# Performance work log

Measured on AMD Instinct MI355X. Metric: run time of the kernel, lower is better.

The kernel has to match this reference:

```python
import jax, jax.numpy as jnp
import numpy as np

N, D, H = 50000, 256, 8
HD = D // H
E = 800000
NEG_SLOPE = 0.2


def setup_inputs() -> dict:
    key = jax.random.key(0)
    ks = jax.random.split(key, 12)
    s = 1.0 / np.sqrt(D)
    return {
        "x": jax.random.normal(ks[0], (N, D), jnp.float32),
        "edge_index": jax.random.randint(ks[1], (2, E), 0, N, jnp.int64),
        "edge_attr": jax.random.normal(ks[2], (E, 16), jnp.float32),
        # GATConv params: lin weight (no bias), attention vectors, output bias
        "W": jax.random.normal(ks[3], (D, D), jnp.float32) * s,
        "att_src": jax.random.normal(ks[4], (H, HD), jnp.float32) * s,
        "att_dst": jax.random.normal(ks[5], (H, HD), jnp.float32) * s,
        "bias": jnp.zeros((D,), jnp.float32),
        # LayerNorm
        "ln_g": jnp.ones((D,), jnp.float32),
        "ln_b": jnp.zeros((D,), jnp.float32),
        # FFN
        "W1": jax.random.normal(ks[6], (D, D), jnp.float32) * s,
        "b1": jnp.zeros((D,), jnp.float32),
        "W2": jax.random.normal(ks[7], (D, D), jnp.float32) * s,
        "b2": jnp.zeros((D,), jnp.float32),
    }


def _gat_layer(x, edge_index, W, att_src, att_dst, bias, ln_g, ln_b, W1, b1, W2, b2):
    n = x.shape[0]
    # GATConv default add_self_loops=True
    sl = jnp.arange(n, dtype=edge_index.dtype)
    src = jnp.concatenate([edge_index[0], sl])  # [E+N]
    dst = jnp.concatenate([edge_index[1], sl])  # [E+N]

    xp = (x @ W).reshape(n, H, HD)                      # [N,H,hd]
    a_src = jnp.einsum("nhd,hd->nh", xp, att_src)        # [N,H]
    a_dst = jnp.einsum("nhd,hd->nh", xp, att_dst)        # [N,H]

    e = a_src[src] + a_dst[dst]                          # [E+N,H]
    e = jax.nn.leaky_relu(e, NEG_SLOPE)
    # segment softmax over destination nodes (every node has a self loop)
    m = jax.ops.segment_max(e, dst, num_segments=n)      # [N,H]
    ex = jnp.exp(e - m[dst])
    denom = jax.ops.segment_sum(ex, dst, num_segments=n) # [N,H]
    alpha = ex / (denom[dst] + 1e-16)                    # [E+N,H]

    msg = alpha[:, :, None] * xp[src]                    # [E+N,H,hd]
    out = jax.ops.segment_sum(msg, dst, num_segments=n)  # [N,H,hd]
    h = out.reshape(n, D) + bias

    # residual + LayerNorm
    r = h + x
    mu = jnp.mean(r, axis=-1, keepdims=True)
    var = jnp.mean(jnp.square(r - mu), axis=-1, keepdims=True)
    hn = (r - mu) / jnp.sqrt(var + 1e-5) * ln_g + ln_b

    # FFN
    return jax.nn.relu(hn @ W1 + b1) @ W2 + b2


def reference(x, edge_index, edge_attr, W, att_src, att_dst, bias, ln_g, ln_b, W1, b1, W2, b2):
    # edge_attr is accepted but unused (GATConv built without edge_dim)
    return _gat_layer(x, edge_index, W, att_src, att_dst, bias, ln_g, ln_b, W1, b1, W2, b2)
```

## Files before the change

kernel.cpp:

```cpp
#include <hip/hip_runtime.h>
#include <hip/hip_bf16.h>

#define H 8
#define HD 32
#define DD 256
#define NEG_SLOPE 0.2f
#define EPB 4096
#define NBMAX 256

typedef short bf16x8 __attribute__((ext_vector_type(8)));
typedef float f32x4 __attribute__((ext_vector_type(4)));

__device__ __forceinline__ unsigned short f2bf(float f) {
    unsigned int u = __float_as_uint(f);
    unsigned int r = (u + 0x7fffu + ((u >> 16) & 1u)) >> 16;
    return (unsigned short)r;
}
__device__ __forceinline__ float bf2f(unsigned short b) {
    return __uint_as_float(((unsigned int)b) << 16);
}

#define GLOAD_LDS16(g, s)                                                        \
    __builtin_amdgcn_global_load_lds((const __attribute__((address_space(1))) void*)(g), \
                                     (__attribute__((address_space(3))) void*)(s), 16, 0, 0)

__global__ __launch_bounds__(256) void zero_gc(int* __restrict__ gc) {
    gc[threadIdx.x] = 0;
}

__global__ __launch_bounds__(256) void prep(const float* __restrict__ x, unsigned short* __restrict__ xb,
                                            const float* __restrict__ W, unsigned short* __restrict__ Wt,
                                            const float* __restrict__ W1, unsigned short* __restrict__ W1t,
                                            const float* __restrict__ W2, unsigned short* __restrict__ W2t,
                                            const int* __restrict__ ei, int* __restrict__ gc,
                                            int* __restrict__ blockBase, int N, int n4, int E, int SB) {
    __shared__ int lhist[NBMAX];
    int b = blockIdx.x;
    int tid = threadIdx.x;
    if (b < SB) {
        lhist[tid] = 0;
        __syncthreads();
        int e0 = b * EPB;
#pragma unroll
        for (int i = 0; i < 16; i++) {
            int e = e0 + i * 256 + tid;
            if (e < E) atomicAdd(&lhist[((unsigned)ei[E + e]) >> 8], 1);
        }
        __syncthreads();
        int c = lhist[tid];
        blockBase[b * NBMAX + tid] = c ? atomicAdd(&gc[tid], c) : 0;
    } else if (b < SB + 768) {
        int wb = b - SB;
        const float* src = (wb < 256) ? W : (wb < 512) ? W1 : W2;
        unsigned short* dst = (wb < 256) ? Wt : (wb < 512) ? W1t : W2t;
        int i = (wb & 255) * 256 + tid;
        int n = i >> 8, k = i & 255;
        dst[i] = f2bf(src[k * 256 + n]);
    } else {
        int i = (b - SB - 768) * 256 + tid;
        if (i < n4) {
            float4 v = ((const float4*)x)[i];
            ushort4 o;
            o.x = f2bf(v.x); o.y = f2bf(v.y); o.z = f2bf(v.z); o.w = f2bf(v.w);
            ((ushort4*)xb)[i] = o;
        }
    }
}

__global__ __launch_bounds__(64) void scan_gc(const int* __restrict__ gc, int* __restrict__ bb) {
    int lane = threadIdx.x;
    int v[4], s = 0;
#pragma unroll
    for (int i = 0; i < 4; i++) { v[i] = gc[lane * 4 + i]; s += v[i]; }
    int sc = s;
#pragma unroll
    for (int off = 1; off < 64; off <<= 1) {
        int t = __shfl_up(sc, off, 64);
        if (lane >= off) sc += t;
    }
    int run = sc - s;
#pragma unroll
    for (int i = 0; i < 4; i++) { bb[lane * 4 + i] = run; run += v[i]; }
}

__global__ __launch_bounds__(256) void bucket_scatter(const int* __restrict__ ei,
                                                      const int* __restrict__ bb,
                                                      const int* __restrict__ blockBase,
                                                      unsigned int* __restrict__ tmp, int E) {
    __shared__ int lrank[NBMAX];
    int b = blockIdx.x;
    int tid = threadIdx.x;
    lrank[tid] = 0;
    __syncthreads();
    int e0 = b * EPB;
#pragma unroll
    for (int i = 0; i < 16; i++) {
        int e = e0 + i * 256 + tid;
        if (e < E) {
            int s = ei[e];
            unsigned d = (unsigned)ei[E + e];
            int k = d >> 8;
            int r = atomicAdd(&lrank[k], 1);
            tmp[bb[k] + blockBase[b * NBMAX + k] + r] = ((d & 255u) << 24) | (unsigned)s;
        }
    }
}

__global__ __launch_bounds__(256) void bucket_csr(const unsigned int* __restrict__ tmp,
                                                  const int* __restrict__ bb, const int* __restrict__ gc,
                                                  int* __restrict__ src_sorted, int* __restrict__ rowPtr,
                                                  int* __restrict__ cnt, int N) {
    __shared__ int dh[NBMAX];
    __shared__ int dbase[NBMAX];
    __shared__ int dr[NBMAX];
    int k = blockIdx.x;
    int tid = threadIdx.x;
    int base = bb[k];
    int M = gc[k];
    dh[tid] = 0;
    dr[tid] = 0;
    __syncthreads();
    for (int i = tid; i < M; i += 256) atomicAdd(&dh[tmp[base + i] >> 24], 1);
    __syncthreads();
    int c = dh[tid];
    dbase[tid] = c;
    __syncthreads();
    for (int off = 1; off < 256; off <<= 1) {
        int add = (tid >= off) ? dbase[tid - off] : 0;
        __syncthreads();
        dbase[tid] += add;
        __syncthreads();
    }
    int excl = dbase[tid] - c;
    int d = (k << 8) + tid;
    if (d < N) { cnt[d] = c; rowPtr[d] = base + excl; }
    __syncthreads();
    dbase[tid] = excl;
    __syncthreads();
    for (int i = tid; i < M; i += 256) {
        unsigned p = tmp[base + i];
        int dl = p >> 24;
        int r = atomicAdd(&dr[dl], 1);
        src_sorted[base + dbase[dl] + r] = (int)(p & 0xFFFFFFu);
    }
}

template <bool ATTN, bool PHASE2>
__global__ __launch_bounds__(256) void gemm_fused(
    const unsigned short* __restrict__ A,
    const unsigned short* __restrict__ B1t, const float* __restrict__ b1,
    const unsigned short* __restrict__ B2t, const float* __restrict__ b2,
    void* __restrict__ Cout, int M,
    const float* __restrict__ att_s, const float* __restrict__ att_d,
    float* __restrict__ a_srcO, float* __restrict__ a_dstO) {
    __shared__ __align__(16) unsigned short Als[16384];
    __shared__ __align__(16) unsigned short t1ls[PHASE2 ? 64 * 280 : 8];

    const int tid = threadIdx.x;
    const int l = tid & 63;
    const int w = tid >> 6;
    const int r16 = l & 15, q0 = l >> 4;
    const int row0 = blockIdx.x * 64;

#pragma unroll
    for (int k = 0; k < 8; k++) {
        int c = k * 256 + tid;
        const unsigned short* g = A + (size_t)min(row0 + (c & 63), M - 1) * DD + (c >> 6) * 8;
        GLOAD_LDS16(g, &Als[c * 8]);
    }
    __syncthreads();

    f32x4 zero = {0.f, 0.f, 0.f, 0.f};
    f32x4 acc[4][4];
#pragma unroll
    for (int i = 0; i < 4; i++)
#pragma unroll
        for (int j = 0; j < 4; j++) acc[i][j] = zero;

#pragma unroll
    for (int kk = 0; kk < 4; kk++) {
#pragma unroll
        for (int t = 0; t < 2; t++) {
            const int qq = kk * 8 + t * 4 + q0;
            bf16x8 af[4], bf[4];
#pragma unroll
            for (int j = 0; j < 4; j++)
                bf[j] = *(const bf16x8*)&B1t[(size_t)(w * 64 + j * 16 + r16) * DD + qq * 8];
#pragma unroll
            for (int i = 0; i < 4; i++)
                af[i] = *(const bf16x8*)&Als[(qq * 64 + i * 16 + r16) * 8];
#pragma unroll
            for (int i = 0; i < 4; i++)
#pragma unroll
                for (int j = 0; j < 4; j++)
                    acc[i][j] = __builtin_amdgcn_mfma_f32_16x16x32_bf16(af[i], bf[j], acc[i][j], 0, 0, 0);
        }
    }

    if (!PHASE2) {
        float aws0, aws1, aws2, aws3, awd0, awd1, awd2, awd3;
        int hA = 0, hB = 0;
        if (ATTN) {
            hA = w * 2; hB = hA + 1;
            aws0 = att_s[hA * HD + r16];
            aws1 = att_s[hA * HD + 16 + r16];
            aws2 = att_s[hB * HD + r16];
            aws3 = att_s[hB * HD + 16 + r16];
            awd0 = att_d[hA * HD + r16];
            awd1 = att_d[hA * HD + 16 + r16];
            awd2 = att_d[hB * HD + r16];
            awd3 = att_d[hB * HD + 16 + r16];
        }
#pragma unroll
        for (int i = 0; i < 4; i++) {
#pragma unroll
            for (int r = 0; r < 4; r++) {
                int row = row0 + i * 16 + q0 * 4 + r;
                if (row < M) {
#pragma unroll
                    for (int j = 0; j < 4; j++) {
                        int col = w * 64 + j * 16 + r16;
                        ((unsigned short*)Cout)[(size_t)row * DD + col] = f2bf(acc[i][j][r]);
                    }
                }
                if (ATTN) {
                    float v0 = acc[i][0][r], v1 = acc[i][1][r];
                    float v2 = acc[i][2][r], v3 = acc[i][3][r];
                    float ps0 = v0 * aws0 + v1 * aws1;
                    float ps1 = v2 * aws2 + v3 * aws3;
                    float pd0 = v0 * awd0 + v1 * awd1;
                    float pd1 = v2 * awd2 + v3 * awd3;
#pragma unroll
                    for (int m = 1; m < 16; m <<= 1) {
                        ps0 += __shfl_xor(ps0, m, 64);
                        ps1 += __shfl_xor(ps1, m, 64);
                        pd0 += __shfl_xor(pd0, m, 64);
                        pd1 += __shfl_xor(pd1, m, 64);
                    }
                    if (r16 == 0 && row < M) {
                        a_srcO[row * H + hA] = ps0;
                        a_srcO[row * H + hB] = ps1;
                        a_dstO[row * H + hA] = pd0;
                        a_dstO[row * H + hB] = pd1;
                    }
                }
            }
        }
    } else {
        float bb1[4];
#pragma unroll
        for (int j = 0; j < 4; j++) bb1[j] = b1[w * 64 + j * 16 + r16];
#pragma unroll
        for (int i = 0; i < 4; i++)
#pragma unroll
            for (int r = 0; r < 4; r++) {
                int rl = i * 16 + q0 * 4 + r;
#pragma unroll
                for (int j = 0; j < 4; j++) {
                    float v = fmaxf(acc[i][j][r] + bb1[j], 0.f);
                    t1ls[rl * 280 + w * 64 + j * 16 + r16] = f2bf(v);
                }
            }
        __syncthreads();

#pragma unroll
        for (int i = 0; i < 4; i++)
#pragma unroll
            for (int j = 0; j < 4; j++) acc[i][j] = zero;

#pragma unroll
        for (int kk = 0; kk < 4; kk++) {
#pragma unroll
            for (int t = 0; t < 2; t++) {
                const int qq = kk * 8 + t * 4 + q0;
                bf16x8 af[4], bf[4];
#pragma unroll
                for (int j = 0; j < 4; j++)
                    bf[j] = *(const bf16x8*)&B2t[(size_t)(w * 64 + j * 16 + r16) * DD + qq * 8];
#pragma unroll
                for (int i = 0; i < 4; i++)
                    af[i] = *(const bf16x8*)&t1ls[(i * 16 + r16) * 280 + qq * 8];
#pragma unroll
                for (int i = 0; i < 4; i++)
#pragma unroll
                    for (int j = 0; j < 4; j++)
                        acc[i][j] = __builtin_amdgcn_mfma_f32_16x16x32_bf16(af[i], bf[j], acc[i][j], 0, 0, 0);
            }
        }

        float bb2[4];
#pragma unroll
        for (int j = 0; j < 4; j++) bb2[j] = b2[w * 64 + j * 16 + r16];
#pragma unroll
        for (int i = 0; i < 4; i++)
#pragma unroll
            for (int r = 0; r < 4; r++) {
                int row = row0 + i * 16 + q0 * 4 + r;
                if (row < M) {
#pragma unroll
                    for (int j = 0; j < 4; j++) {
                        int col = w * 64 + j * 16 + r16;
                        ((float*)Cout)[(size_t)row * DD + col] = acc[i][j][r] + bb2[j];
                    }
                }
            }
    }
}

__global__ __launch_bounds__(256) void aggregate_ln(
    const unsigned short* __restrict__ xp, const unsigned short* __restrict__ x_bf,
    const float* __restrict__ a_src, const float* __restrict__ a_dst,
    const int* __restrict__ rowPtr, const int* __restrict__ cnt,
    const int* __restrict__ src_sorted,
    const float* __restrict__ bias, const float* __restrict__ ln_g,
    const float* __restrict__ ln_b, unsigned short* __restrict__ hn, int N) {
    int wave = threadIdx.x >> 6;
    int lane = threadIdx.x & 63;
    int n = blockIdx.x * 4 + wave;
    if (n >= N) return;
    int h = lane >> 3;

    float adst = a_dst[n * H + h];
    float e0 = a_src[n * H + h] + adst;
    e0 = (e0 > 0.f) ? e0 : NEG_SLOPE * e0;
    float ex = __expf(e0);
    ushort4 u = *(const ushort4*)(xp + (size_t)n * DD + lane * 4);
    float acc0 = ex * bf2f(u.x), acc1 = ex * bf2f(u.y);
    float acc2 = ex * bf2f(u.z), acc3 = ex * bf2f(u.w);
    float denom = ex;

    int beg = rowPtr[n];
    int end = beg + cnt[n];
    int i = beg;
    for (; i + 7 < end; i += 8) {
        int s[8];
        float es[8];
        ushort4 uu[8];
#pragma unroll
        for (int k = 0; k < 8; k++) s[k] = src_sorted[i + k];
#pragma unroll
        for (int k = 0; k < 8; k++) es[k] = a_src[s[k] * H + h];
#pragma unroll
        for (int k = 0; k < 8; k++) uu[k] = *(const ushort4*)(xp + (size_t)s[k] * DD + lane * 4);
#pragma unroll
        for (int k = 0; k < 8; k++) {
            float e = es[k] + adst;
            e = (e > 0.f) ? e : NEG_SLOPE * e;
            float wk = __expf(e);
            acc0 += wk * bf2f(uu[k].x);
            acc1 += wk * bf2f(uu[k].y);
            acc2 += wk * bf2f(uu[k].z);
            acc3 += wk * bf2f(uu[k].w);
            denom += wk;
        }
    }
    for (; i < end; i++) {
        int s0 = src_sorted[i];
        float es0 = a_src[s0 * H + h];
        ushort4 u0 = *(const ushort4*)(xp + (size_t)s0 * DD + lane * 4);
        float e0a = es0 + adst;
        e0a = (e0a > 0.f) ? e0a : NEG_SLOPE * e0a;
        float w0 = __expf(e0a);
        acc0 += w0 * bf2f(u0.x);
        acc1 += w0 * bf2f(u0.y);
        acc2 += w0 * bf2f(u0.z);
        acc3 += w0 * bf2f(u0.w);
        denom += w0;
    }
    float inv = 1.f / (denom + 1e-16f);
    float4 bb = *(const float4*)(bias + lane * 4);
    ushort4 xr = *(const ushort4*)(x_bf + (size_t)n * DD + lane * 4);
    float r0 = acc0 * inv + bb.x + bf2f(xr.x);
    float r1 = acc1 * inv + bb.y + bf2f(xr.y);
    float r2 = acc2 * inv + bb.z + bf2f(xr.z);
    float r3 = acc3 * inv + bb.w + bf2f(xr.w);

    float s = r0 + r1 + r2 + r3;
#pragma unroll
    for (int m = 1; m < 64; m <<= 1) s += __shfl_xor(s, m, 64);
    float mu = s * (1.f / 256.f);
    float d0 = r0 - mu, d1 = r1 - mu, d2 = r2 - mu, d3 = r3 - mu;
    float qv = d0 * d0 + d1 * d1 + d2 * d2 + d3 * d3;
#pragma unroll
    for (int m = 1; m < 64; m <<= 1) qv += __shfl_xor(qv, m, 64);
    float rstd = rsqrtf(qv * (1.f / 256.f) + 1e-5f);
    float4 g = *(const float4*)(ln_g + lane * 4);
    float4 b = *(const float4*)(ln_b + lane * 4);
    ushort4 o;
    o.x = f2bf(d0 * rstd * g.x + b.x);
    o.y = f2bf(d1 * rstd * g.y + b.y);
    o.z = f2bf(d2 * rstd * g.z + b.z);
    o.w = f2bf(d3 * rstd * g.w + b.w);
    *(ushort4*)(hn + (size_t)n * DD + lane * 4) = o;
}

extern "C" void kernel_launch(void* const* d_in, const int* in_sizes, int n_in,
                              void* d_out, int out_size, void* d_ws, size_t ws_size,
                              hipStream_t stream) {
    const float* x = (const float*)d_in[0];
    const int* edge_index = (const int*)d_in[1];
    const float* W = (const float*)d_in[3];
    const float* att_src = (const float*)d_in[4];
    const float* att_dst = (const float*)d_in[5];
    const float* bias = (const float*)d_in[6];
    const float* ln_g = (const float*)d_in[7];
    const float* ln_b = (const float*)d_in[8];
    const float* W1 = (const float*)d_in[9];
    const float* b1 = (const float*)d_in[10];
    const float* W2 = (const float*)d_in[11];
    const float* b2 = (const float*)d_in[12];

    const int N = in_sizes[0] / DD;
    const int E = in_sizes[1] / 2;

    char* p = (char*)d_ws;
    auto carve = [&](size_t bytes) {
        char* r = p;
        p += (bytes + 255) & ~(size_t)255;
        return r;
    };
    unsigned short* x_bf = (unsigned short*)carve((size_t)N * DD * 2);
    unsigned short* xp_bf = (unsigned short*)carve((size_t)N * DD * 2);
    unsigned short* hn_bf = (unsigned short*)carve((size_t)N * DD * 2);
    float* a_src = (float*)carve((size_t)N * H * 4);
    float* a_dst = (float*)carve((size_t)N * H * 4);
    int* gc = (int*)carve(NBMAX * 4);
    int* bb = (int*)carve(NBMAX * 4);
    int* rowPtr = (int*)carve((size_t)N * 4);
    int* cnt = (int*)carve((size_t)N * 4);
    unsigned int* tmp = (unsigned int*)carve((size_t)E * 4);
    int* src_sorted = (int*)carve((size_t)E * 4);
    int* blockBase = (int*)carve((size_t)((E + EPB - 1) / EPB) * NBMAX * 4);
    unsigned short* Wt = (unsigned short*)carve(65536 * 2);
    unsigned short* W1t = (unsigned short*)carve(65536 * 2);
    unsigned short* W2t = (unsigned short*)carve(65536 * 2);

    const int n4 = N * DD / 4;
    const int SB = (E + EPB - 1) / EPB;
    const int NB = (N + 255) >> 8;

    zero_gc<<<1, 256, 0, stream>>>(gc);

    int prep_blocks = SB + 768 + (n4 + 255) / 256;
    prep<<<prep_blocks, 256, 0, stream>>>(x, x_bf, W, Wt, W1, W1t, W2, W2t,
                                          edge_index, gc, blockBase, N, n4, E, SB);

    scan_gc<<<1, 64, 0, stream>>>(gc, bb);
    bucket_scatter<<<SB, 256, 0, stream>>>(edge_index, bb, blockBase, tmp, E);
    bucket_csr<<<NB, 256, 0, stream>>>(tmp, bb, gc, src_sorted, rowPtr, cnt, N);

    const int gblocks = (N + 63) / 64;

    gemm_fused<true, false><<<gblocks, 256, 0, stream>>>(
        x_bf, Wt, nullptr, nullptr, nullptr, xp_bf, N, att_src, att_dst, a_src, a_dst);

    aggregate_ln<<<(N + 3) / 4, 256, 0, stream>>>(xp_bf, x_bf, a_src, a_dst, rowPtr, cnt,
                                                  src_sorted, bias, ln_g, ln_b, hn_bf, N);

    gemm_fused<false, true><<<gblocks, 256, 0, stream>>>(
        hn_bf, W1t, b1, W2t, b2, d_out, N, nullptr, nullptr, nullptr, nullptr);
}
```

Baseline: 331.1 us.

## Drop global-counter atomics and merge CSR build into first GEMM launch

The prep kernel now writes raw per-block bucket histograms, and each consumer block recomputes its bucket offsets by summing and scanning those histograms, so the zero, atomic and scan_gc steps go away. The per-bucket CSR construction moves into extra blocks appended to the first fused GEMM launch, so it runs alongside the projection GEMM. Together this removes three kernel launches and the global atomics. The cost is redundant work: every scatter block loops over all SB histogram rows, and the GEMM kernel gets a divergent branch and more parameters.

```diff
diff --git a/kernel.cpp b/kernel.cpp
--- a/kernel.cpp
+++ b/kernel.cpp
@@ -24,16 +24,29 @@
     __builtin_amdgcn_global_load_lds((const __attribute__((address_space(1))) void*)(g), \
                                      (__attribute__((address_space(3))) void*)(s), 16, 0, 0)
 
-__global__ __launch_bounds__(256) void zero_gc(int* __restrict__ gc) {
-    gc[threadIdx.x] = 0;
+__device__ __forceinline__ int block_excl_scan(int v, int* wp) {
+    int tid = threadIdx.x, lane = tid & 63, wv = tid >> 6;
+    int s = v;
+#pragma unroll
+    for (int off = 1; off < 64; off <<= 1) {
+        int t = __shfl_up(s, off, 64);
+        if (lane >= off) s += t;
+    }
+    __syncthreads();
+    if (lane == 63) wp[wv] = s;
+    __syncthreads();
+    int wbase = 0;
+#pragma unroll
+    for (int i = 0; i < 4; i++) wbase += (i < wv) ? wp[i] : 0;
+    return wbase + s - v;
 }
 
 __global__ __launch_bounds__(256) void prep(const float* __restrict__ x, unsigned short* __restrict__ xb,
                                             const float* __restrict__ W, unsigned short* __restrict__ Wt,
                                             const float* __restrict__ W1, unsigned short* __restrict__ W1t,
                                             const float* __restrict__ W2, unsigned short* __restrict__ W2t,
-                                            const int* __restrict__ ei, int* __restrict__ gc,
-                                            int* __restrict__ blockBase, int N, int n4, int E, int SB) {
+                                            const int* __restrict__ ei, int* __restrict__ blockBase,
+                                            int N, int n4, int E, int SB) {
     __shared__ int lhist[NBMAX];
     int b = blockIdx.x;
     int tid = threadIdx.x;
@@ -47,8 +60,7 @@
             if (e < E) atomicAdd(&lhist[((unsigned)ei[E + e]) >> 8], 1);
         }
         __syncthreads();
-        int c = lhist[tid];
-        blockBase[b * NBMAX + tid] = c ? atomicAdd(&gc[tid], c) : 0;
+        blockBase[b * NBMAX + tid] = lhist[tid];
     } else if (b < SB + 768) {
         int wb = b - SB;
         const float* src = (wb < 256) ? W : (wb < 512) ? W1 : W2;
@@ -67,29 +79,22 @@
     }
 }
 
-__global__ __launch_bounds__(64) void scan_gc(const int* __restrict__ gc, int* __restrict__ bb) {
-    int lane = threadIdx.x;
-    int v[4], s = 0;
-#pragma unroll
-    for (int i = 0; i < 4; i++) { v[i] = gc[lane * 4 + i]; s += v[i]; }
-    int sc = s;
-#pragma unroll
-    for (int off = 1; off < 64; off <<= 1) {
-        int t = __shfl_up(sc, off, 64);
-        if (lane >= off) sc += t;
-    }
-    int run = sc - s;
-#pragma unroll
-    for (int i = 0; i < 4; i++) { bb[lane * 4 + i] = run; run += v[i]; }
-}
-
 __global__ __launch_bounds__(256) void bucket_scatter(const int* __restrict__ ei,
-                                                      const int* __restrict__ bb,
                                                       const int* __restrict__ blockBase,
-                                                      unsigned int* __restrict__ tmp, int E) {
+                                                      unsigned int* __restrict__ tmp, int E, int SB) {
+    __shared__ int myb[NBMAX];
     __shared__ int lrank[NBMAX];
+    __shared__ int wp[4];
     int b = blockIdx.x;
     int tid = threadIdx.x;
+    int t = 0, pb = 0;
+    for (int bb = 0; bb < SB; bb++) {
+        int c = blockBase[bb * NBMAX + tid];
+        t += c;
+        if (bb < b) pb += c;
+    }
+    int excl = block_excl_scan(t, wp);
+    myb[tid] = excl + pb;
     lrank[tid] = 0;
     __syncthreads();
     int e0 = b * EPB;
@@ -101,47 +106,8 @@
             unsigned d = (unsigned)ei[E + e];
             int k = d >> 8;
             int r = atomicAdd(&lrank[k], 1);
-            tmp[bb[k] + blockBase[b * NBMAX + k] + r] = ((d & 255u) << 24) | (unsigned)s;
-        }
-    }
-}
-
-__global__ __launch_bounds__(256) void bucket_csr(const unsigned int* __restrict__ tmp,
-                                                  const int* __restrict__ bb, const int* __restrict__ gc,
-                                                  int* __restrict__ src_sorted, int* __restrict__ rowPtr,
-                                                  int* __restrict__ cnt, int N) {
-    __shared__ int dh[NBMAX];
-    __shared__ int dbase[NBMAX];
-    __shared__ int dr[NBMAX];
-    int k = blockIdx.x;
-    int tid = threadIdx.x;
-    int base = bb[k];
-    int M = gc[k];
-    dh[tid] = 0;
-    dr[tid] = 0;
-    __syncthreads();
-    for (int i = tid; i < M; i += 256) atomicAdd(&dh[tmp[base + i] >> 24], 1);
-    __syncthreads();
-    int c = dh[tid];
-    dbase[tid] = c;
-    __syncthreads();
-    for (int off = 1; off < 256; off <<= 1) {
-        int add = (tid >= off) ? dbase[tid - off] : 0;
-        __syncthreads();
-        dbase[tid] += add;
-        __syncthreads();
-    }
-    int excl = dbase[tid] - c;
-    int d = (k << 8) + tid;
-    if (d < N) { cnt[d] = c; rowPtr[d] = base + excl; }
-    __syncthreads();
-    dbase[tid] = excl;
-    __syncthreads();
-    for (int i = tid; i < M; i += 256) {
-        unsigned p = tmp[base + i];
-        int dl = p >> 24;
-        int r = atomicAdd(&dr[dl], 1);
-        src_sorted[base + dbase[dl] + r] = (int)(p & 0xFFFFFFu);
+            tmp[myb[k] + r] = ((d & 255u) << 24) | (unsigned)s;
+        }
     }
 }
 
@@ -152,11 +118,53 @@
     const unsigned short* __restrict__ B2t, const float* __restrict__ b2,
     void* __restrict__ Cout, int M,
     const float* __restrict__ att_s, const float* __restrict__ att_d,
-    float* __restrict__ a_srcO, float* __restrict__ a_dstO) {
+    float* __restrict__ a_srcO, float* __restrict__ a_dstO,
+    const int* __restrict__ blockBase, const unsigned int* __restrict__ tmp,
+    int* __restrict__ src_sorted, int* __restrict__ rowPtr, int* __restrict__ cnt,
+    int N, int SB, int gB) {
     __shared__ __align__(16) unsigned short Als[16384];
     __shared__ __align__(16) unsigned short t1ls[PHASE2 ? 64 * 280 : 8];
 
     const int tid = threadIdx.x;
+
+    if constexpr (ATTN) {
+        if ((int)blockIdx.x >= gB) {
+            int k = (int)blockIdx.x - gB;
+            int* L = (int*)Als;
+            int* exclArr = L;
+            int* totArr = L + 256;
+            int* dh = L + 512;
+            int* dbase = L + 768;
+            int* dr = L + 1024;
+            int* wp = L + 1280;
+            int t = 0;
+            for (int b = 0; b < SB; b++) t += blockBase[b * NBMAX + tid];
+            int excl = block_excl_scan(t, wp);
+            exclArr[tid] = excl;
+            totArr[tid] = t;
+            dh[tid] = 0;
+            dr[tid] = 0;
+            __syncthreads();
+            int base = exclArr[k];
+            int M_ = totArr[k];
+            for (int i = tid; i < M_; i += 256) atomicAdd(&dh[tmp[base + i] >> 24], 1);
+            __syncthreads();
+            int c = dh[tid];
+            int dexcl = block_excl_scan(c, wp);
+            int d = (k << 8) + tid;
+            if (d < N) { cnt[d] = c; rowPtr[d] = base + dexcl; }
+            dbase[tid] = dexcl;
+            __syncthreads();
+            for (int i = tid; i < M_; i += 256) {
+                unsigned p = tmp[base + i];
+                int dl = p >> 24;
+                int r = atomicAdd(&dr[dl], 1);
+                src_sorted[base + dbase[dl] + r] = (int)(p & 0xFFFFFFu);
+            }
+            return;
+        }
+    }
+
     const int l = tid & 63;
     const int w = tid >> 6;
     const int r16 = l & 15, q0 = l >> 4;
@@ -424,8 +432,6 @@
     unsigned short* hn_bf = (unsigned short*)carve((size_t)N * DD * 2);
     float* a_src = (float*)carve((size_t)N * H * 4);
     float* a_dst = (float*)carve((size_t)N * H * 4);
-    int* gc = (int*)carve(NBMAX * 4);
-    int* bb = (int*)carve(NBMAX * 4);
     int* rowPtr = (int*)carve((size_t)N * 4);
     int* cnt = (int*)carve((size_t)N * 4);
     unsigned int* tmp = (unsigned int*)carve((size_t)E * 4);
@@ -439,24 +445,22 @@
     const int SB = (E + EPB - 1) / EPB;
     const int NB = (N + 255) >> 8;
 
-    zero_gc<<<1, 256, 0, stream>>>(gc);
-
     int prep_blocks = SB + 768 + (n4 + 255) / 256;
     prep<<<prep_blocks, 256, 0, stream>>>(x, x_bf, W, Wt, W1, W1t, W2, W2t,
-                                          edge_index, gc, blockBase, N, n4, E, SB);
-
-    scan_gc<<<1, 64, 0, stream>>>(gc, bb);
-    bucket_scatter<<<SB, 256, 0, stream>>>(edge_index, bb, blockBase, tmp, E);
-    bucket_csr<<<NB, 256, 0, stream>>>(tmp, bb, gc, src_sorted, rowPtr, cnt, N);
+                                          edge_index, blockBase, N, n4, E, SB);
+
+    bucket_scatter<<<SB, 256, 0, stream>>>(edge_index, blockBase, tmp, E, SB);
 
     const int gblocks = (N + 63) / 64;
 
-    gemm_fused<true, false><<<gblocks, 256, 0, stream>>>(
-        x_bf, Wt, nullptr, nullptr, nullptr, xp_bf, N, att_src, att_dst, a_src, a_dst);
+    gemm_fused<true, false><<<gblocks + NB, 256, 0, stream>>>(
+        x_bf, Wt, nullptr, nullptr, nullptr, xp_bf, N, att_src, att_dst, a_src, a_dst,
+        blockBase, tmp, src_sorted, rowPtr, cnt, N, SB, gblocks);
 
     aggregate_ln<<<(N + 3) / 4, 256, 0, stream>>>(xp_bf, x_bf, a_src, a_dst, rowPtr, cnt,
                                                   src_sorted, bias, ln_g, ln_b, hn_bf, N);
 
     gemm_fused<false, true><<<gblocks, 256, 0, stream>>>(
-        hn_bf, W1t, b1, W2t, b2, d_out, N, nullptr, nullptr, nullptr, nullptr);
-}
+        hn_bf, W1t, b1, W2t, b2, d_out, N, nullptr, nullptr, nullptr, nullptr,
+        nullptr, nullptr, nullptr, nullptr, nullptr, 0, 0, gblocks);
+}
```

New measurement: 363.2 us. +9.7%, slower.
